# Performance work log

Measured on AMD Instinct MI355X. Metric: run time of the kernel, lower is better.

Reference implementation:

```python
import jax, jax.numpy as jnp
import numpy as np

M = 150000  # number of nodes
K = 64      # neighbor_limits[-1]


def setup_inputs() -> dict:
    key = jax.random.key(0)
    k1, k2 = jax.random.split(key)
    nodes = jax.random.normal(k1, (M, 3), dtype=jnp.float32)
    # radius_search-style neighbor table: values in [0, M], where index == M is padding
    node_knn_indices = jax.random.randint(k2, (M, K), 0, M + 1, dtype=jnp.int64)
    return {"nodes": nodes, "node_knn_indices": node_knn_indices}


def _greedy_nms(knn):
    # Sequential greedy suppression: node i is kept iff none of its radius
    # neighbors with smaller index was already kept. masks has size M+1 so the
    # padding index M always reads False (never suppresses).
    m = knn.shape[0]
    masks0 = jnp.zeros(m + 1, dtype=bool)

    def step(masks, xs):
        i, row = xs
        keep = ~jnp.any(masks[row])  # masks[node_knn_indices[i]].sum() == 0
        return masks.at[i].set(keep), None

    masks, _ = jax.lax.scan(step, masks0, (jnp.arange(m), knn))
    return masks


def reference(nodes, node_knn_indices):
    masks = _greedy_nms(node_knn_indices)
    kept = masks[:-1]  # [M] bool
    # Original returns node_knn_indices[kept] (data-dependent shape). For a
    # jit-compatible fixed shape we return the full table with suppressed rows
    # overwritten by the padding index M; kept rows are bitwise identical.
    m = node_knn_indices.shape[0]
    kept_knn = jnp.where(kept[:, None], node_knn_indices, m)
    return kept, kept_knn
```

## Files before the change

### kernel.cpp

```cpp
#include <hip/hip_runtime.h>


#define M_ROWS 150000
#define KNN    64
#define BLK    1024
#define QRT    2
#define CHUNK  (BLK * QRT)
#define NCH    ((M_ROWS + CHUNK - 1) / CHUNK)
#define ICAP   6
#define ECAP   16
#define WCH    8
#define W64PC  (CHUNK / 32)
#define LMW    (((NCH - 1) * CHUNK) / 32)
#define NBMG   ((NCH - 1) * W64PC)
#define OUT_INTS (M_ROWS + M_ROWS * KNN)
#define BMG_INT_OFF (OUT_INTS - NBMG * 2)
#define DECFULL 0xffffffffu

__global__ void init_ws_kernel(unsigned int* progress, int* out) {
  const int i = blockIdx.x * blockDim.x + threadIdx.x;
  unsigned long long* bmg64 = (unsigned long long*)(out + BMG_INT_OFF);
  if (i < NBMG) bmg64[i] = 0ull;
  if (i == 0) *progress = 0u;
}

__device__ __forceinline__ bool probe_reload(const int* __restrict__ rp,
                                             const unsigned int* lm,
                                             int lo, int hi) {
  bool s = false;
#pragma unroll
  for (int u = 0; u < 16; ++u) {
    int4 d = ((const int4*)rp)[u];
    int js[4] = {d.x, d.y, d.z, d.w};
#pragma unroll
    for (int m = 0; m < 4; ++m) {
      int j = js[m];
      if (j >= lo && j < hi && ((lm[j >> 5] >> (j & 31)) & 1u)) s = true;
    }
  }
  return s;
}

__global__ __launch_bounds__(BLK) void nms_chain_kernel(
    const int* __restrict__ knn,
    int* __restrict__ out,
    unsigned int* __restrict__ progress)
{
  const int b    = blockIdx.x;
  const int t    = threadIdx.x;
  const int base = b * CHUNK;
  const int winb = (b > WCH) ? (base - WCH * CHUNK) : 0;

  unsigned long long* bmg64 = (unsigned long long*)(out + BMG_INT_OFF);

  __shared__ unsigned char      st[CHUNK];
  __shared__ unsigned short     il[ICAP][CHUNK];
  __shared__ unsigned short     exl[ECAP][CHUNK];
  __shared__ unsigned int       lm[LMW];
  __shared__ unsigned int       sh_p;

  int  rowq[QRT];
  bool vq[QRT], ovf[QRT], eovf[QRT], supp[QRT];
  int  ic[QRT], ec[QRT];

#pragma unroll
  for (int q = 0; q < QRT; ++q) {
    rowq[q] = base + q * BLK + t;
    vq[q]   = rowq[q] < M_ROWS;
    ic[q] = ec[q] = 0;
    ovf[q] = eovf[q] = supp[q] = false;
  }

#pragma unroll
  for (int q = 0; q < QRT; ++q) {
    if (!vq[q]) continue;
    const int o   = q * BLK + t;
    const int row = rowq[q];
    const int* rp = knn + (long long)row * KNN;
#pragma unroll
    for (int u = 0; u < 16; ++u) {
      int4 d = ((const int4*)rp)[u];
      int js[4] = {d.x, d.y, d.z, d.w};
#pragma unroll
      for (int m = 0; m < 4; ++m) {
        int j = js[m];
        if (j < row) {
          if (j >= base) {
            if (ic[q] < ICAP) il[ic[q]][o] = (unsigned short)(j - base);
            ++ic[q];
          } else if (j >= winb) {
            if (ec[q] < ECAP) exl[ec[q]][o] = (unsigned short)(j - winb);
            ++ec[q];
          }
        }
      }
    }
  }
#pragma unroll
  for (int q = 0; q < QRT; ++q) {
    ovf[q]  = ic[q] > ICAP; if (ovf[q])  ic[q] = ICAP;
    eovf[q] = ec[q] > ECAP; if (eovf[q]) ec[q] = ECAP;
  }

  unsigned short ilr[QRT][ICAP];
#pragma unroll
  for (int q = 0; q < QRT; ++q)
#pragma unroll
    for (int x = 0; x < ICAP; ++x)
      ilr[q][x] = il[x][q * BLK + t];

  int praw1 = 0;
  if (b > WCH) {
    if (t < 64) {
      int pr = 0;
      for (int spin = 0; spin < (1 << 22); ++spin) {
        pr = (int)__hip_atomic_load(progress, __ATOMIC_RELAXED,
                                    __HIP_MEMORY_SCOPE_AGENT);
        if (pr >= b - WCH) break;
        __builtin_amdgcn_s_sleep(2);
      }
      if (t == 0) sh_p = (unsigned int)pr;
    }
    __syncthreads();
    praw1 = (int)sh_p; if (praw1 > b) praw1 = b;
    const int wt = praw1 * W64PC;
    for (int w = t; w < wt; w += BLK) {
      unsigned long long v = __hip_atomic_load(&bmg64[w], __ATOMIC_RELAXED,
                                               __HIP_MEMORY_SCOPE_AGENT);
      int g1 = 0;
      while (((unsigned int)(v >> 32)) != DECFULL && ++g1 < (1 << 22)) {
        __builtin_amdgcn_s_sleep(1);
        v = __hip_atomic_load(&bmg64[w], __ATOMIC_RELAXED,
                              __HIP_MEMORY_SCOPE_AGENT);
      }
      lm[w] = (unsigned int)v;
    }
    __syncthreads();
    const int lim = praw1 * CHUNK;
#pragma unroll
    for (int q = 0; q < QRT; ++q)
      if (vq[q])
        supp[q] = probe_reload(knn + (long long)rowq[q] * KNN, lm, 0, lim);
  }
  const int pr1lim = praw1 * CHUNK;

  unsigned int extm[QRT];
  bool eunk[QRT];
#pragma unroll
  for (int q = 0; q < QRT; ++q) {
    extm[q] = 0u; eunk[q] = false;
    if (vq[q] && !supp[q]) {
      const int o = q * BLK + t;
      const int n = ec[q];
#pragma unroll
      for (int x = 0; x < ECAP; ++x) {
        if (x < n) {
          const int j = winb + (int)exl[x][o];
          if (j >= pr1lim) extm[q] |= (1u << x);
        }
      }
      eunk[q] = eovf[q];
    }
  }

  unsigned char myst[QRT];
#pragma unroll
  for (int q = 0; q < QRT; ++q) {
    myst[q] = (!vq[q] || supp[q]) ? (unsigned char)2
            : ((ic[q] == 0 && !ovf[q] && extm[q] == 0u && !eunk[q])
               ? (unsigned char)1 : (unsigned char)0);
    __hip_atomic_store(&st[q * BLK + t], myst[q],
                       __ATOMIC_RELAXED, __HIP_MEMORY_SCOPE_WORKGROUP);
  }
  __syncthreads();

  const int lane = t & 63;
  const bool pub = (b < NCH - 1);
  if (pub) {
#pragma unroll
    for (int q = 0; q < QRT; ++q) {
      unsigned long long bdec  = __ballot(myst[q] != 0);
      unsigned long long bkept = __ballot(myst[q] == 1);
      const int g = b * W64PC + ((q * BLK + (t & ~63)) >> 5);
      if (lane == 0)
        (void)__hip_atomic_fetch_or(&bmg64[g],
            ((bdec & 0xffffffffull) << 32) | (bkept & 0xffffffffull),
            __ATOMIC_RELAXED, __HIP_MEMORY_SCOPE_AGENT);
      if (lane == 32)
        (void)__hip_atomic_fetch_or(&bmg64[g + 1],
            ((bdec >> 32) << 32) | (bkept >> 32),
            __ATOMIC_RELAXED, __HIP_MEMORY_SCOPE_AGENT);
    }
  }

  bool undec = false;
#pragma unroll
  for (int q = 0; q < QRT; ++q) undec |= (myst[q] == 0);

  for (int pass = 0; pass < (1 << 22); ++pass) {
    bool pend = false;
    if (undec) {
#pragma unroll
      for (int q = 0; q < QRT; ++q) {
        if (myst[q] != 0) continue;
        const int o   = q * BLK + t;
        const int row = base + o;
        bool anyK = false, allD = true;
        unsigned int m = extm[q];

        if (m != 0u) {
#pragma unroll
          for (int g = 0; g < 2; ++g) {
            if ((m >> (g * 8)) & 0xffu) {
              unsigned long long vv[8];
#pragma unroll
              for (int x = 0; x < 8; ++x) {
                const int xe = g * 8 + x;
                const int j = winb + (int)exl[xe][o];
                const int w = ((m >> xe) & 1u) ? (j >> 5) : 0;
                vv[x] = __hip_atomic_load(&bmg64[w], __ATOMIC_RELAXED,
                                          __HIP_MEMORY_SCOPE_AGENT);
              }
#pragma unroll
              for (int x = 0; x < 8; ++x) {
                const int xe = g * 8 + x;
                if ((m >> xe) & 1u) {
                  const int j = winb + (int)exl[xe][o];
                  const int bit = j & 31;
                  if ((((unsigned int)(vv[x] >> 32)) >> bit) & 1u) {
                    if ((((unsigned int)vv[x]) >> bit) & 1u) anyK = true;
                    m &= ~(1u << xe);
                  } else pend = true;
                }
              }
            }
          }
          extm[q] = m;
        }

        if (!ovf[q]) {
          unsigned char vsts[ICAP];
#pragma unroll
          for (int x = 0; x < ICAP; ++x) {
            const int ii = (x < ic[q]) ? (int)ilr[q][x] : 0;
            vsts[x] = __hip_atomic_load(&st[ii],
                __ATOMIC_RELAXED, __HIP_MEMORY_SCOPE_WORKGROUP);
          }
#pragma unroll
          for (int x = 0; x < ICAP; ++x) {
            if (x < ic[q]) { anyK |= (vsts[x] == 1); allD &= (vsts[x] != 0); }
          }
        } else {
          const int* rp = knn + (long long)row * KNN;
#pragma unroll
          for (int u = 0; u < 16; ++u) {
            int4 d = ((const int4*)rp)[u];
            int js[4] = {d.x, d.y, d.z, d.w};
            unsigned char sv[4];
#pragma unroll
            for (int m2 = 0; m2 < 4; ++m2) {
              const bool in = (js[m2] >= base && js[m2] < row);
              sv[m2] = __hip_atomic_load(&st[in ? (js[m2] - base) : 0],
                  __ATOMIC_RELAXED, __HIP_MEMORY_SCOPE_WORKGROUP);
            }
#pragma unroll
            for (int m2 = 0; m2 < 4; ++m2) {
              if (js[m2] >= base && js[m2] < row) {
                anyK |= (sv[m2] == 1); allD &= (sv[m2] != 0);
              }
            }
          }
        }
        if (extm[q] != 0u) allD = false;

        if (!anyK && eunk[q]) {
          const int lo = (pr1lim > winb) ? pr1lim : winb;
          const int* rp = knn + (long long)row * KNN;
          bool ep = false, ak = false;
#pragma unroll
          for (int g = 0; g < 8; ++g) {
            int js[8];
#pragma unroll
            for (int u = 0; u < 2; ++u) {
              int4 d = ((const int4*)rp)[g * 2 + u];
              js[u * 4 + 0] = d.x; js[u * 4 + 1] = d.y;
              js[u * 4 + 2] = d.z; js[u * 4 + 3] = d.w;
            }
            unsigned long long wv[8];
#pragma unroll
            for (int m2 = 0; m2 < 8; ++m2) {
              const bool in = (js[m2] >= lo && js[m2] < base);
              wv[m2] = __hip_atomic_load(&bmg64[in ? (js[m2] >> 5) : 0],
                  __ATOMIC_RELAXED, __HIP_MEMORY_SCOPE_AGENT);
            }
#pragma unroll
            for (int m2 = 0; m2 < 8; ++m2) {
              if (js[m2] >= lo && js[m2] < base) {
                const int bit = js[m2] & 31;
                if ((((unsigned int)(wv[m2] >> 32)) >> bit) & 1u) {
                  if ((((unsigned int)wv[m2]) >> bit) & 1u) ak = true;
                } else ep = true;
              }
            }
          }
          if (ak) anyK = true;
          else if (!ep) eunk[q] = false;
          if (ep) pend = true;
        }
        if (eunk[q]) allD = false;

        if (anyK)      myst[q] = 2;
        else if (allD) myst[q] = 1;
        if (myst[q] != 0) {
          __hip_atomic_store(&st[o], myst[q],
                             __ATOMIC_RELAXED, __HIP_MEMORY_SCOPE_WORKGROUP);
          if (pub) {
            const int g = b * W64PC + (o >> 5);
            const int bit = o & 31;
            unsigned long long val = (1ull << (32 + bit))
                | ((myst[q] == 1) ? (1ull << bit) : 0ull);
            (void)__hip_atomic_fetch_or(&bmg64[g], val,
                __ATOMIC_RELAXED, __HIP_MEMORY_SCOPE_AGENT);
          }
        }
      }

#pragma unroll
      for (int s = 0; s < 2; ++s) {
#pragma unroll
        for (int q = 0; q < QRT; ++q) {
          if (myst[q] != 0 || ovf[q]) continue;
          const int o = q * BLK + t;
          bool anyK = false, allD = true;
          unsigned char vsts[ICAP];
#pragma unroll
          for (int x = 0; x < ICAP; ++x) {
            const int ii = (x < ic[q]) ? (int)ilr[q][x] : 0;
            vsts[x] = __hip_atomic_load(&st[ii],
                __ATOMIC_RELAXED, __HIP_MEMORY_SCOPE_WORKGROUP);
          }
#pragma unroll
          for (int x = 0; x < ICAP; ++x) {
            if (x < ic[q]) { anyK |= (vsts[x] == 1); allD &= (vsts[x] != 0); }
          }
          if (extm[q] != 0u || eunk[q]) allD = false;
          if (anyK)      myst[q] = 2;
          else if (allD) myst[q] = 1;
          if (myst[q] != 0) {
            __hip_atomic_store(&st[o], myst[q],
                               __ATOMIC_RELAXED, __HIP_MEMORY_SCOPE_WORKGROUP);
            if (pub) {
              const int g = b * W64PC + (o >> 5);
              const int bit = o & 31;
              unsigned long long val = (1ull << (32 + bit))
                  | ((myst[q] == 1) ? (1ull << bit) : 0ull);
              (void)__hip_atomic_fetch_or(&bmg64[g], val,
                  __ATOMIC_RELAXED, __HIP_MEMORY_SCOPE_AGENT);
            }
          }
        }
      }

      undec = false;
#pragma unroll
      for (int q = 0; q < QRT; ++q) undec |= (myst[q] == 0);
    }

    if (__ballot(undec) == 0ull) break;
    if (__ballot(pend) != 0ull) __builtin_amdgcn_s_sleep(1);
  }

  if (pub) {
#pragma unroll
    for (int q = 0; q < QRT; ++q) {
      unsigned long long bkept = __ballot(myst[q] == 1);
      const int g = b * W64PC + ((q * BLK + (t & ~63)) >> 5);
      if (lane == 0)
        __hip_atomic_store(&bmg64[g],
            (0xffffffffull << 32) | (bkept & 0xffffffffull),
            __ATOMIC_RELAXED, __HIP_MEMORY_SCOPE_AGENT);
      if (lane == 32)
        __hip_atomic_store(&bmg64[g + 1],
            (0xffffffffull << 32) | (bkept >> 32),
            __ATOMIC_RELAXED, __HIP_MEMORY_SCOPE_AGENT);
    }
  }
  __syncthreads();
  if (t == 0)
    __hip_atomic_store(progress, (unsigned int)(b + 1),
                       __ATOMIC_RELAXED, __HIP_MEMORY_SCOPE_AGENT);

  bool kq[QRT];
#pragma unroll
  for (int q = 0; q < QRT; ++q)
    kq[q] = vq[q] && (myst[q] == 1);

#pragma unroll
  for (int q = 0; q < QRT; ++q)
    if (vq[q]) out[rowq[q]] = kq[q] ? 1 : 0;

#pragma unroll
  for (int q = 0; q < QRT; ++q) {
    if (!vq[q]) continue;
    const int row = rowq[q];
    const int* rp = knn + (long long)row * KNN;
    int* orow = out + M_ROWS + (long long)row * KNN;
    const bool k = kq[q];
#pragma unroll
    for (int u = 0; u < 16; ++u) {
      int4 d = ((const int4*)rp)[u];
      int4 o4;
      o4.x = k ? d.x : M_ROWS;
      o4.y = k ? d.y : M_ROWS;
      o4.z = k ? d.z : M_ROWS;
      o4.w = k ? d.w : M_ROWS;
      ((int4*)orow)[u] = o4;
    }
  }
}

extern "C" void kernel_launch(void* const* d_in, const int* in_sizes, int n_in,
                              void* d_out, int out_size, void* d_ws, size_t ws_size,
                              hipStream_t stream) {
  const int* knn = (const int*)d_in[1];
  int* out = (int*)d_out;
  unsigned int* progress = (unsigned int*)d_ws;

  init_ws_kernel<<<(NBMG + BLK - 1) / BLK, BLK, 0, stream>>>(progress, out);
  nms_chain_kernel<<<NCH, BLK, 0, stream>>>(knn, out, progress);
}
```

Measured before the change: 420.8 us.

## Replace progress store with done counter and widen dependency window

Blocks now publish completion by atomically incrementing a shared done counter with release semantics, replacing the per-block progress store. The last block waits until every other block has finished before it writes output, because the bitmap region overlaps the output buffer. The window of preceding chunks that is waited on grows from 8 to 16, and the per-row external-neighbor list capacity grows from 16 to 24 with a third probe group. The goal is fewer overflow fallbacks and less serialized waiting, in exchange for more shared memory, a count-based progress check that can be satisfied out of order, and a tail barrier on the last block.

```diff
diff --git a/kernel.cpp b/kernel.cpp
--- a/kernel.cpp
+++ b/kernel.cpp
@@ -8,8 +8,8 @@
 #define CHUNK  (BLK * QRT)
 #define NCH    ((M_ROWS + CHUNK - 1) / CHUNK)
 #define ICAP   6
-#define ECAP   16
-#define WCH    8
+#define ECAP   24
+#define WCH    16
 #define W64PC  (CHUNK / 32)
 #define LMW    (((NCH - 1) * CHUNK) / 32)
 #define NBMG   ((NCH - 1) * W64PC)
@@ -17,11 +17,11 @@
 #define BMG_INT_OFF (OUT_INTS - NBMG * 2)
 #define DECFULL 0xffffffffu
 
-__global__ void init_ws_kernel(unsigned int* progress, int* out) {
+__global__ void init_ws_kernel(unsigned int* done, int* out) {
   const int i = blockIdx.x * blockDim.x + threadIdx.x;
   unsigned long long* bmg64 = (unsigned long long*)(out + BMG_INT_OFF);
   if (i < NBMG) bmg64[i] = 0ull;
-  if (i == 0) *progress = 0u;
+  if (i == 0) *done = 0u;
 }
 
 __device__ __forceinline__ bool probe_reload(const int* __restrict__ rp,
@@ -44,7 +44,7 @@
 __global__ __launch_bounds__(BLK) void nms_chain_kernel(
     const int* __restrict__ knn,
     int* __restrict__ out,
-    unsigned int* __restrict__ progress)
+    unsigned int* __restrict__ done)
 {
   const int b    = blockIdx.x;
   const int t    = threadIdx.x;
@@ -114,7 +114,7 @@
     if (t < 64) {
       int pr = 0;
       for (int spin = 0; spin < (1 << 22); ++spin) {
-        pr = (int)__hip_atomic_load(progress, __ATOMIC_RELAXED,
+        pr = (int)__hip_atomic_load(done, __ATOMIC_RELAXED,
                                     __HIP_MEMORY_SCOPE_AGENT);
         if (pr >= b - WCH) break;
         __builtin_amdgcn_s_sleep(2);
@@ -210,7 +210,7 @@
 
         if (m != 0u) {
 #pragma unroll
-          for (int g = 0; g < 2; ++g) {
+          for (int g = 0; g < 3; ++g) {
             if ((m >> (g * 8)) & 0xffu) {
               unsigned long long vv[8];
 #pragma unroll
@@ -370,6 +370,7 @@
     if (__ballot(pend) != 0ull) __builtin_amdgcn_s_sleep(1);
   }
 
+  __syncthreads();
   if (pub) {
 #pragma unroll
     for (int q = 0; q < QRT; ++q) {
@@ -386,9 +387,21 @@
     }
   }
   __syncthreads();
-  if (t == 0)
-    __hip_atomic_store(progress, (unsigned int)(b + 1),
-                       __ATOMIC_RELAXED, __HIP_MEMORY_SCOPE_AGENT);
+  if (pub && t == 0)
+    (void)__hip_atomic_fetch_add(done, 1u,
+        __ATOMIC_RELEASE, __HIP_MEMORY_SCOPE_AGENT);
+
+  if (b == NCH - 1) {
+    if (t < 64) {
+      for (int spin = 0; spin < (1 << 22); ++spin) {
+        unsigned int dv = __hip_atomic_load(done, __ATOMIC_ACQUIRE,
+                                            __HIP_MEMORY_SCOPE_AGENT);
+        if (dv >= (unsigned int)(NCH - 1)) break;
+        __builtin_amdgcn_s_sleep(2);
+      }
+    }
+    __syncthreads();
+  }
 
   bool kq[QRT];
 #pragma unroll
@@ -424,8 +437,8 @@
                               hipStream_t stream) {
   const int* knn = (const int*)d_in[1];
   int* out = (int*)d_out;
-  unsigned int* progress = (unsigned int*)d_ws;
-
-  init_ws_kernel<<<(NBMG + BLK - 1) / BLK, BLK, 0, stream>>>(progress, out);
-  nms_chain_kernel<<<NCH, BLK, 0, stream>>>(knn, out, progress);
+  unsigned int* done = (unsigned int*)d_ws;
+
+  init_ws_kernel<<<(NBMG + BLK - 1) / BLK, BLK, 0, stream>>>(done, out);
+  nms_chain_kernel<<<NCH, BLK, 0, stream>>>(knn, out, done);
 }
```

Result: faster. 364.2 us (-13.5%).
